# Kernel tuning notes

Hardware: AMD Instinct MI355X
Metric: run time of the kernel (lower is better)

## Reference

```python
import jax, jax.numpy as jnp
import numpy as np

N_HEADS = 16


def _rotate_half(x):
    x_even = x[..., ::2]
    x_odd = x[..., 1::2]
    return jnp.stack((-x_odd, x_even), axis=-1).reshape(x.shape)


def _apply_rope(x, cos, sin):
    # cos/sin: (S, d_head) broadcast against (B, H, S, d_head)
    return x * cos + _rotate_half(x) * sin


def setup_inputs() -> dict:
    key = jax.random.key(0)
    k1, k2, k3 = jax.random.split(key, 3)
    B, S, D, H = 2, 2048, 1024, N_HEADS
    dh = D // H
    x = jax.random.normal(k1, (B, S, D), dtype=jnp.float32)
    w_qkv = jax.random.normal(k2, (D, 3 * D), dtype=jnp.float32) * 0.02
    w_proj = jax.random.normal(k3, (D, D), dtype=jnp.float32) * 0.02
    # standard interleaved RoPE tables, shape (S, d_head)
    inv_freq = 1.0 / (10000.0 ** (jnp.arange(0, dh, 2, dtype=jnp.float32) / dh))
    angles = jnp.arange(S, dtype=jnp.float32)[:, None] * inv_freq[None, :]  # (S, dh/2)
    rope_cos = jnp.repeat(jnp.cos(angles), 2, axis=-1)  # (S, dh)
    rope_sin = jnp.repeat(jnp.sin(angles), 2, axis=-1)
    return {"x": x, "w_qkv": w_qkv, "w_proj": w_proj, "rope_cos": rope_cos, "rope_sin": rope_sin}


def reference(x, w_qkv, w_proj, rope_cos, rope_sin):
    B, S, D = x.shape
    H = N_HEADS
    dh = D // H
    half = dh // 2
    qkv = x @ w_qkv  # (B, S, 3D)
    q, k, v = jnp.split(qkv, 3, axis=-1)
    # (B, S, D) -> (B, H, S, dh)
    q = q.reshape(B, S, H, dh).transpose(0, 2, 1, 3)
    k = k.reshape(B, S, H, dh).transpose(0, 2, 1, 3)
    v = v.reshape(B, S, H, dh).transpose(0, 2, 1, 3)
    q = _apply_rope(q, rope_cos, rope_sin)
    k = _apply_rope(k, rope_cos, rope_sin)
    scale = half ** -0.5
    # dual score matrices from the two half-subspaces
    attn_up = jnp.einsum('bhid,bhjd->bhij', q[..., :half], k[..., :half]) * scale
    attn_down = jnp.einsum('bhid,bhjd->bhij', q[..., half:], k[..., half:]) * scale
    lower_mask = jnp.tril(jnp.ones((S, S), dtype=bool))  # j <= i -> down
    attn_logits = jnp.where(lower_mask, attn_down, attn_up)
    attn_weights = jax.nn.softmax(attn_logits, axis=-1)
    attn_out = jnp.einsum('bhij,bhjd->bhid', attn_weights, v)
    attn_out = attn_out.transpose(0, 2, 1, 3).reshape(B, S, D)
    return attn_out @ w_proj
```

## Files before the change

kernel.cpp:

```cpp
#include <hip/hip_runtime.h>
#include <hip/hip_bf16.h>
#include <stdint.h>

typedef __bf16 bf16;
typedef __attribute__((ext_vector_type(4))) __bf16 bf16x4;
typedef __attribute__((ext_vector_type(8))) __bf16 bf16x8;
typedef __attribute__((ext_vector_type(4))) float f32x4;

#define MFMA16(a, b, c) __builtin_amdgcn_mfma_f32_16x16x32_bf16((a), (b), (c), 0, 0, 0)

#define QSC (0.17677669529663687f * 1.4426950408889634f)

__device__ __forceinline__ void async_cp16(const bf16* g, bf16* l) {
  __builtin_amdgcn_global_load_lds(
      (const __attribute__((address_space(1))) void*)g,
      (__attribute__((address_space(3))) void*)l, 16, 0, 0);
}

__global__ __launch_bounds__(256) void convx_k(const float* __restrict__ in,
                                               bf16* __restrict__ out, int n) {
  int i = (blockIdx.x * 256 + threadIdx.x) * 4;
  const int stride = gridDim.x * 256 * 4;
  for (; i < n; i += stride) {
    const f32x4 f = *(const f32x4*)(in + i);
    bf16x4 o;
    o[0] = (bf16)f[0]; o[1] = (bf16)f[1]; o[2] = (bf16)f[2]; o[3] = (bf16)f[3];
    *(bf16x4*)(out + i) = o;
  }
}

__global__ __launch_bounds__(256) void transpose_k(const float* __restrict__ in,
                                                   bf16* __restrict__ out, int R, int C) {
  __shared__ bf16 t[64][65];
  const int bc = blockIdx.x * 64;
  const int br = blockIdx.y * 64;
  const int tx = threadIdx.x & 63, ty = threadIdx.x >> 6;
#pragma unroll
  for (int r = ty; r < 64; r += 4) t[r][tx] = (bf16)in[(br + r) * C + bc + tx];
  __syncthreads();
#pragma unroll
  for (int r = ty; r < 64; r += 4) out[(bc + r) * R + br + tx] = t[tx][r];
}

template <int MODE, int BM>
__global__ __launch_bounds__(256) void gemm128(
    const bf16* __restrict__ A, const bf16* __restrict__ BT, int M, int N, int K,
    float* __restrict__ C, bf16* __restrict__ qws, bf16* __restrict__ kws,
    bf16* __restrict__ vT, const float* __restrict__ ropeC, const float* __restrict__ ropeS) {
  constexpr int MT = BM / 32;
  __shared__ __align__(16) bf16 As[BM * 32];
  __shared__ __align__(16) bf16 Bs[128 * 32];
  const int tid = threadIdx.x;
  const int lane = tid & 63, wave = tid >> 6;
  const int l16 = lane & 15, quad = lane >> 4;
  const int wm = (wave >> 1) * (BM / 2), wn = (wave & 1) * 64;
  const int bm = blockIdx.y, bn = blockIdx.x;

  const bf16* ag = A + (bm * BM + (tid >> 2)) * K + (tid & 3) * 8;
  const bf16* bg = BT + (bn * 128 + (tid >> 2)) * K + (tid & 3) * 8;
  bf16* la = &As[tid * 8];
  bf16* lb = &Bs[tid * 8];

  f32x4 acc[MT][4] = {};

  for (int k0 = 0; k0 < K; k0 += 32) {
    async_cp16(ag + k0, la);
    if (BM == 128) async_cp16(ag + 64 * K + k0, la + 2048);
    async_cp16(bg + k0, lb);
    async_cp16(bg + 64 * K + k0, lb + 2048);
    __syncthreads();
    bf16x8 af[MT], bff[4];
#pragma unroll
    for (int t = 0; t < MT; ++t)
      af[t] = *(const bf16x8*)&As[(wm + t * 16 + l16) * 32 + quad * 8];
#pragma unroll
    for (int t = 0; t < 4; ++t)
      bff[t] = *(const bf16x8*)&Bs[(wn + t * 16 + l16) * 32 + quad * 8];
#pragma unroll
    for (int mt = 0; mt < MT; ++mt)
#pragma unroll
      for (int nt = 0; nt < 4; ++nt) acc[mt][nt] = MFMA16(af[mt], bff[nt], acc[mt][nt]);
    __syncthreads();
  }

  if (MODE == 0) {
#pragma unroll
    for (int mt = 0; mt < MT; ++mt)
#pragma unroll
      for (int i = 0; i < 4; ++i) {
        const int row = bm * BM + wm + mt * 16 + quad * 4 + i;
#pragma unroll
        for (int nt = 0; nt < 4; ++nt) {
          const int col = bn * 128 + wn + nt * 16 + l16;
          C[row * N + col] = acc[mt][nt][i];
        }
      }
  } else {
    bf16* tb = &Bs[wave * 512];
#pragma unroll
    for (int mt = 0; mt < MT; ++mt) {
      const int s0 = bm * BM + wm + mt * 16;
      const int b = s0 >> 11, sbase = s0 & 2047;
#pragma unroll
      for (int nt = 0; nt < 4; ++nt) {
        const int colb = bn * 128 + wn + nt * 16;
        const int sec = colb >> 10, rem = colb & 1023;
        const int h = rem >> 6, d0 = rem & 63;
        if (sec < 2) {
          const int d = d0 + l16;
#pragma unroll
          for (int i = 0; i < 4; ++i) {
            const int s = sbase + quad * 4 + i;
            float v = acc[mt][nt][i];
            float pr = __shfl_xor(v, 1);
            float rot = (d & 1) ? pr : -pr;
            float rv = v * ropeC[s * 64 + d] + rot * ropeS[s * 64 + d];
            if (sec == 0) rv *= QSC;
            tb[(quad * 4 + i) * 20 + l16] = (bf16)rv;
          }
          bf16* dst = ((sec == 0) ? qws : kws) + ((b * 16 + h) * 2048 + sbase) * 64 + d0;
          bf16x4 seg = *(const bf16x4*)&tb[l16 * 20 + quad * 4];
          *(bf16x4*)(dst + l16 * 64 + quad * 4) = seg;
        } else {
          const int d = d0 + l16;
          const int s4 = sbase + quad * 4;
          const int a = (s4 >> 4) & 3;
          const int p = (s4 & ~63) | ((a >> 1) * 32 + quad * 8 + (a & 1) * 4);
          bf16x4 pk;
#pragma unroll
          for (int i = 0; i < 4; ++i) pk[i] = (bf16)acc[mt][nt][i];
          *(bf16x4*)(vT + ((b * 16 + h) * 64 + d) * 2048 + p) = pk;
        }
      }
    }
  }
}

__global__ __launch_bounds__(256) void attn_k(const bf16* __restrict__ qws,
                                              const bf16* __restrict__ kws,
                                              const bf16* __restrict__ vT,
                                              bf16* __restrict__ aw) {
  __shared__ __align__(16) bf16 Ks[2][64 * 64];
  __shared__ __align__(16) bf16 Vs[2][64 * 64];
  const int tid = threadIdx.x;
  const int lane = tid & 63, wave = tid >> 6;
  const int l16 = lane & 15, quad = lane >> 4;
  const int bh = blockIdx.x >> 4, qblk = blockIdx.x & 15;
  const int b = bh >> 4, h = bh & 15;
  const int rbase = qblk * 128 + wave * 32;

  const bf16* qb = qws + (bh * 2048 + rbase) * 64;
  const bf16* kb = kws + bh * 2048 * 64;
  const bf16* vb = vT + bh * 64 * 2048;

  const int r0 = wave * 16 + (lane >> 3);
  const int c0 = ((lane & 7) - r0) & 7;
  const bf16* kst0 = kb + r0 * 64 + c0 * 8;
  const bf16* kst1 = kb + (r0 + 8) * 64 + c0 * 8;
  const bf16* vst0 = vb + r0 * 2048 + c0 * 8;
  const bf16* vst1 = vb + (r0 + 8) * 2048 + c0 * 8;

#define STAGE(jtv)                                         \
  {                                                        \
    bf16* kdst = &Ks[(jtv) & 1][wave * 1024];              \
    bf16* vdst = &Vs[(jtv) & 1][wave * 1024];              \
    async_cp16(kst0 + (jtv) * 4096, kdst);                 \
    async_cp16(kst1 + (jtv) * 4096, kdst + 512);           \
    async_cp16(vst0 + (jtv) * 64, vdst);                   \
    async_cp16(vst1 + (jtv) * 64, vdst + 512);             \
  }

  bf16x8 qf[2][2];
#pragma unroll
  for (int g = 0; g < 2; ++g)
#pragma unroll
    for (int hf = 0; hf < 2; ++hf)
      qf[g][hf] = *(const bf16x8*)(qb + (g * 16 + l16) * 64 + hf * 32 + quad * 8);

  f32x4 o[2][4] = {};
  float lp[2] = {0.f, 0.f};
  const f32x4 zz = {};
  const int tdw = rbase >> 6;

#define ATTN_BODY(TM, jt)                                                             \
  {                                                                                   \
    const bf16* Kb = Ks[(jt) & 1];                                                    \
    const bf16* Vb = Vs[(jt) & 1];                                                    \
    bf16x8 vf[2][4];                                                                  \
    _Pragma("unroll") for (int ks = 0; ks < 2; ++ks)                                  \
      _Pragma("unroll") for (int ntd = 0; ntd < 4; ++ntd)                             \
        vf[ks][ntd] = *(const bf16x8*)(Vb + (ntd * 16 + l16) * 64 +                   \
                                       ((ks * 4 + quad + l16) & 7) * 8);              \
    bf16x8 kfU[2][2], kfD[2][2];                                                      \
    _Pragma("unroll") for (int ks = 0; ks < 2; ++ks)                                  \
      _Pragma("unroll") for (int s = 0; s < 2; ++s) {                                 \
        const int ro = ((ks * 2 + s) * 16 + l16) * 64;                                \
        if (TM != 0) kfU[ks][s] = *(const bf16x8*)(Kb + ro + ((quad + l16) & 7) * 8); \
        if (TM != 2)                                                                  \
          kfD[ks][s] = *(const bf16x8*)(Kb + ro + ((4 + quad + l16) & 7) * 8);        \
      }                                                                               \
    if ((jt) + 1 < 32) STAGE((jt) + 1)                                                \
    _Pragma("unroll") for (int ks = 0; ks < 2; ++ks) {                                \
      f32x4 sU[2][2], sD[2][2];                                                       \
      _Pragma("unroll") for (int s = 0; s < 2; ++s)                                   \
        _Pragma("unroll") for (int g = 0; g < 2; ++g) {                               \
          if (TM != 0) sU[s][g] = MFMA16(kfU[ks][s], qf[g][0], zz);                   \
          if (TM != 2) sD[s][g] = MFMA16(kfD[ks][s], qf[g][1], zz);                   \
        }                                                                             \
      _Pragma("unroll") for (int g = 0; g < 2; ++g) {                                 \
        bf16x8 af;                                                                    \
        float ls = 0.f;                                                               \
        _Pragma("unroll") for (int s = 0; s < 2; ++s)                                 \
          _Pragma("unroll") for (int r = 0; r < 4; ++r) {                             \
            float x;                                                                  \
            if (TM == 0) x = sD[s][g][r];                                             \
            else if (TM == 2) x = sU[s][g][r];                                        \
            else {                                                                    \
              const int jcol = (jt) * 64 + (ks * 2 + s) * 16 + quad * 4 + r;          \
              x = (jcol <= rbase + g * 16 + l16) ? sD[s][g][r] : sU[s][g][r];         \
            }                                                                         \
            float pe = exp2f(x);                                                      \
            ls += pe;                                                                 \
            af[s * 4 + r] = (bf16)pe;                                                 \
          }                                                                           \
        lp[g] += ls;                                                                  \
        _Pragma("unroll") for (int ntd = 0; ntd < 4; ++ntd)                           \
            o[g][ntd] = MFMA16(af, vf[ks][ntd], o[g][ntd]);                           \
      }                                                                               \
    }                                                                                 \
  }

  STAGE(0)
  for (int jt = 0; jt < 32; ++jt) {
    asm volatile("s_waitcnt vmcnt(0)" ::: "memory");
    __syncthreads();
    if (jt < tdw) ATTN_BODY(0, jt)
    else if (jt == tdw) ATTN_BODY(1, jt)
    else ATTN_BODY(2, jt)
  }
#undef ATTN_BODY
#undef STAGE

#pragma unroll
  for (int g = 0; g < 2; ++g) {
    lp[g] += __shfl_xor(lp[g], 16);
    lp[g] += __shfl_xor(lp[g], 32);
  }
#pragma unroll
  for (int g = 0; g < 2; ++g) {
    float ir[4];
#pragma unroll
    for (int r = 0; r < 4; ++r) ir[r] = 1.0f / __shfl(lp[g], quad * 4 + r);
#pragma unroll
    for (int ntd = 0; ntd < 4; ++ntd)
#pragma unroll
      for (int r = 0; r < 4; ++r)
        aw[(b * 2048 + rbase + g * 16 + quad * 4 + r) * 1024 + h * 64 + ntd * 16 + l16] =
            (bf16)(o[g][ntd][r] * ir[r]);
  }
}

extern "C" void kernel_launch(void* const* d_in, const int* in_sizes, int n_in,
                              void* d_out, int out_size, void* d_ws, size_t ws_size,
                              hipStream_t stream) {
  const float* x = (const float*)d_in[0];
  const float* w_qkv = (const float*)d_in[1];
  const float* w_proj = (const float*)d_in[2];
  const float* ropeC = (const float*)d_in[3];
  const float* ropeS = (const float*)d_in[4];
  float* out = (float*)d_out;

  char* ws = (char*)d_ws;
  bf16* xb = (bf16*)ws;     ws += (size_t)4194304 * 2;
  bf16* wqkvT = (bf16*)ws;  ws += (size_t)3145728 * 2;
  bf16* wprojT = (bf16*)ws; ws += (size_t)1048576 * 2;
  bf16* qws = (bf16*)ws;    ws += (size_t)4194304 * 2;
  bf16* kws = (bf16*)ws;    ws += (size_t)4194304 * 2;
  bf16* vT = (bf16*)ws;     ws += (size_t)4194304 * 2;
  bf16* aw = (bf16*)ws;     ws += (size_t)4194304 * 2;

  convx_k<<<1024, 256, 0, stream>>>(x, xb, 4194304);
  transpose_k<<<dim3(3072 / 64, 1024 / 64), 256, 0, stream>>>(w_qkv, wqkvT, 1024, 3072);
  transpose_k<<<dim3(1024 / 64, 1024 / 64), 256, 0, stream>>>(w_proj, wprojT, 1024, 1024);

  gemm128<1, 128><<<dim3(3072 / 128, 4096 / 128), 256, 0, stream>>>(
      xb, wqkvT, 4096, 3072, 1024, nullptr, qws, kws, vT, ropeC, ropeS);
  attn_k<<<512, 256, 0, stream>>>(qws, kws, vT, aw);
  gemm128<0, 64><<<dim3(1024 / 128, 4096 / 64), 256, 0, stream>>>(
      aw, wprojT, 4096, 1024, 1024, out, nullptr, nullptr, nullptr, nullptr, nullptr);
}
```

Baseline: 216.1 us.

## Double GEMM K-tile with swizzled LDS; compute softmax row sums via MFMA

The GEMM main loop now stages 64-wide K slices instead of 32, halving the number of barrier pairs per tile. It uses an XOR-style chunk rotation in LDS to avoid bank conflicts. In attention, the softmax denominator is accumulated by an extra MFMA against a ones vector instead of scalar adds and cross-lane shuffles. It also uses the raw exp2 and rcp intrinsics. These trade slightly more LDS and MFMA work, and bf16-rounded probabilities in the sum, for fewer VALU ops and syncs.

```diff
diff --git a/kernel.cpp b/kernel.cpp
--- a/kernel.cpp
+++ b/kernel.cpp
@@ -48,38 +48,53 @@
     float* __restrict__ C, bf16* __restrict__ qws, bf16* __restrict__ kws,
     bf16* __restrict__ vT, const float* __restrict__ ropeC, const float* __restrict__ ropeS) {
   constexpr int MT = BM / 32;
-  __shared__ __align__(16) bf16 As[BM * 32];
-  __shared__ __align__(16) bf16 Bs[128 * 32];
+  __shared__ __align__(16) bf16 As[BM * 64];
+  __shared__ __align__(16) bf16 Bs[128 * 64];
   const int tid = threadIdx.x;
   const int lane = tid & 63, wave = tid >> 6;
   const int l16 = lane & 15, quad = lane >> 4;
   const int wm = (wave >> 1) * (BM / 2), wn = (wave & 1) * 64;
   const int bm = blockIdx.y, bn = blockIdx.x;
 
-  const bf16* ag = A + (bm * BM + (tid >> 2)) * K + (tid & 3) * 8;
-  const bf16* bg = BT + (bn * 128 + (tid >> 2)) * K + (tid & 3) * 8;
+  const int srow = tid >> 3;
+  const int schunk = ((tid & 7) - srow) & 7;
+  const bf16* ag = A + (bm * BM + srow) * K + schunk * 8;
+  const bf16* bg = BT + (bn * 128 + srow) * K + schunk * 8;
   bf16* la = &As[tid * 8];
   bf16* lb = &Bs[tid * 8];
 
   f32x4 acc[MT][4] = {};
 
-  for (int k0 = 0; k0 < K; k0 += 32) {
+  for (int k0 = 0; k0 < K; k0 += 64) {
     async_cp16(ag + k0, la);
-    if (BM == 128) async_cp16(ag + 64 * K + k0, la + 2048);
+    async_cp16(ag + 32 * K + k0, la + 2048);
+    if (BM == 128) {
+      async_cp16(ag + 64 * K + k0, la + 4096);
+      async_cp16(ag + 96 * K + k0, la + 6144);
+    }
     async_cp16(bg + k0, lb);
-    async_cp16(bg + 64 * K + k0, lb + 2048);
+    async_cp16(bg + 32 * K + k0, lb + 2048);
+    async_cp16(bg + 64 * K + k0, lb + 4096);
+    async_cp16(bg + 96 * K + k0, lb + 6144);
     __syncthreads();
-    bf16x8 af[MT], bff[4];
-#pragma unroll
-    for (int t = 0; t < MT; ++t)
-      af[t] = *(const bf16x8*)&As[(wm + t * 16 + l16) * 32 + quad * 8];
-#pragma unroll
-    for (int t = 0; t < 4; ++t)
-      bff[t] = *(const bf16x8*)&Bs[(wn + t * 16 + l16) * 32 + quad * 8];
-#pragma unroll
-    for (int mt = 0; mt < MT; ++mt)
-#pragma unroll
-      for (int nt = 0; nt < 4; ++nt) acc[mt][nt] = MFMA16(af[mt], bff[nt], acc[mt][nt]);
+#pragma unroll
+    for (int ks = 0; ks < 2; ++ks) {
+      bf16x8 af[MT], bff[4];
+#pragma unroll
+      for (int t = 0; t < MT; ++t) {
+        const int r = wm + t * 16 + l16;
+        af[t] = *(const bf16x8*)&As[r * 64 + ((ks * 4 + quad + r) & 7) * 8];
+      }
+#pragma unroll
+      for (int t = 0; t < 4; ++t) {
+        const int r = wn + t * 16 + l16;
+        bff[t] = *(const bf16x8*)&Bs[r * 64 + ((ks * 4 + quad + r) & 7) * 8];
+      }
+#pragma unroll
+      for (int mt = 0; mt < MT; ++mt)
+#pragma unroll
+        for (int nt = 0; nt < 4; ++nt) acc[mt][nt] = MFMA16(af[mt], bff[nt], acc[mt][nt]);
+    }
     __syncthreads();
   }
 
@@ -177,8 +192,12 @@
     for (int hf = 0; hf < 2; ++hf)
       qf[g][hf] = *(const bf16x8*)(qb + (g * 16 + l16) * 64 + hf * 32 + quad * 8);
 
+  bf16x8 ones;
+#pragma unroll
+  for (int j = 0; j < 8; ++j) ones[j] = (bf16)1.0f;
+
   f32x4 o[2][4] = {};
-  float lp[2] = {0.f, 0.f};
+  f32x4 o_l[2] = {};
   const f32x4 zz = {};
   const int tdw = rbase >> 6;
 
@@ -209,7 +228,6 @@
         }                                                                             \
       _Pragma("unroll") for (int g = 0; g < 2; ++g) {                                 \
         bf16x8 af;                                                                    \
-        float ls = 0.f;                                                               \
         _Pragma("unroll") for (int s = 0; s < 2; ++s)                                 \
           _Pragma("unroll") for (int r = 0; r < 4; ++r) {                             \
             float x;                                                                  \
@@ -219,11 +237,9 @@
               const int jcol = (jt) * 64 + (ks * 2 + s) * 16 + quad * 4 + r;          \
               x = (jcol <= rbase + g * 16 + l16) ? sD[s][g][r] : sU[s][g][r];         \
             }                                                                         \
-            float pe = exp2f(x);                                                      \
-            ls += pe;                                                                 \
-            af[s * 4 + r] = (bf16)pe;                                                 \
+            af[s * 4 + r] = (bf16)__builtin_amdgcn_exp2f(x);                          \
           }                                                                           \
-        lp[g] += ls;                                                                  \
+        o_l[g] = MFMA16(af, ones, o_l[g]);                                            \
         _Pragma("unroll") for (int ntd = 0; ntd < 4; ++ntd)                           \
             o[g][ntd] = MFMA16(af, vf[ks][ntd], o[g][ntd]);                           \
       }                                                                               \
@@ -243,14 +259,9 @@
 
 #pragma unroll
   for (int g = 0; g < 2; ++g) {
-    lp[g] += __shfl_xor(lp[g], 16);
-    lp[g] += __shfl_xor(lp[g], 32);
-  }
-#pragma unroll
-  for (int g = 0; g < 2; ++g) {
     float ir[4];
 #pragma unroll
-    for (int r = 0; r < 4; ++r) ir[r] = 1.0f / __shfl(lp[g], quad * 4 + r);
+    for (int r = 0; r < 4; ++r) ir[r] = __builtin_amdgcn_rcpf(o_l[g][r]);
 #pragma unroll
     for (int ntd = 0; ntd < 4; ++ntd)
 #pragma unroll
```

Result: faster. 196.0 us (-9.3%).
